# Optimization experiments

Hardware: AMD Instinct MI355X
Metric: run time of the kernel (lower is better)

The kernel has to match this reference:

```python
import jax, jax.numpy as jnp
import numpy as np

M, K, N = 8192, 4096, 4096  # tokens, in_features, out_features

def setup_inputs() -> dict:
    key = jax.random.key(0)
    k1, k2, k3 = jax.random.split(key, 3)
    x = jax.random.normal(k1, (M, K), dtype=jnp.float32)
    # kaiming_uniform_(a=sqrt(5)) on [out,in] -> uniform(-1/sqrt(in), 1/sqrt(in))
    bound = 1.0 / np.sqrt(K)
    weight = jax.random.uniform(k2, (N, K), dtype=jnp.float32, minval=-bound, maxval=bound)
    bias = jax.random.uniform(k3, (N,), dtype=jnp.float32, minval=-bound, maxval=bound)
    return {
        "x": x,
        "weight": weight,
        "bias": bias,
        "input_scale": jnp.float32(1.0),
        "weight_scale": jnp.float32(1.0),
    }


def reference(x, weight, bias, input_scale, weight_scale):
    # Quantize input and weight to fp8 e4m3 (per-tensor scale = 1.0 in module),
    # then dequant-matmul: out = (x_fp8 @ w_fp8^T) * scale_a * scale_b + bias,
    # matching torch._scaled_mm semantics with out_dtype=float32.
    x_fp8 = x.astype(jnp.float8_e4m3fn)
    w_fp8 = weight.astype(jnp.float8_e4m3fn)
    out = jnp.einsum(
        "mk,nk->mn",
        x_fp8.astype(jnp.float32),
        w_fp8.astype(jnp.float32),
    ) * (input_scale * weight_scale)
    return out + bias[None, :]
```

## Files before the change

### kernel.cpp

```cpp
#include <hip/hip_runtime.h>
#include <hip/hip_fp8.h>
#include <cstdint>

typedef float f32x4 __attribute__((ext_vector_type(4)));
typedef int i32x8 __attribute__((ext_vector_type(8)));
typedef long long i64;

static constexpr int Mdim = 8192;
static constexpr int Kdim = 4096;
static constexpr int Ndim = 4096;

static constexpr int BM = 256, BN = 256, BK = 128;
static constexpr int NT = Kdim / BK;
static constexpr int NWG_M = Mdim / BM;
static constexpr int NWG_N = Ndim / BN;
static constexpr int NWG = NWG_M * NWG_N;


__device__ __forceinline__ uint8_t f32_to_e4m3(float f) {
  return (uint8_t)__hip_cvt_float_to_fp8(f, __HIP_SATFINITE, __HIP_E4M3);
}

__device__ __forceinline__ uint4 cvt16(const float4 f0, const float4 f1,
                                       const float4 f2, const float4 f3) {
  const float v[16] = {f0.x, f0.y, f0.z, f0.w, f1.x, f1.y, f1.z, f1.w,
                       f2.x, f2.y, f2.z, f2.w, f3.x, f3.y, f3.z, f3.w};
  union alignas(16) {
    uint32_t u[4];
    uint8_t b[16];
    uint4 q;
  } r;
#pragma unroll
  for (int j = 0; j < 16; ++j) r.b[j] = f32_to_e4m3(v[j]);
  return r.q;
}

__global__ __launch_bounds__(256) void quant_fp8_kernel(
    const float* __restrict__ in, uint8_t* __restrict__ out, int n_vec16) {
  const int stride = gridDim.x * blockDim.x;
  for (int i = blockIdx.x * blockDim.x + threadIdx.x; i < n_vec16; i += stride) {
    const float4* src = reinterpret_cast<const float4*>(in) + (size_t)i * 4;
    reinterpret_cast<uint4*>(out)[i] = cvt16(src[0], src[1], src[2], src[3]);
  }
}

__global__ __launch_bounds__(256) void quant_pack_w_kernel(
    const float* __restrict__ W, uint8_t* __restrict__ PB) {
  const int stride = gridDim.x * blockDim.x;
  const int total = (Ndim / 16) * (Kdim / 16) * 16;
  for (int t = blockIdx.x * blockDim.x + threadIdx.x; t < total; t += stride) {
    const int g = t >> 8;
    const int kbi = t & 255;
    const int kt = kbi >> 3;
    const int kq = (kbi >> 1) & 3;
    const int h = kbi & 1;
    const int rb = g >> 4, r15 = g & 15;
    const float4* src =
        reinterpret_cast<const float4*>(W + (size_t)g * Kdim + kbi * 16);
    const size_t o = (((size_t)(rb * 32 + kt) * 2 + h) * 4 + kq) * 16 + r15;
    reinterpret_cast<uint4*>(PB)[o] = cvt16(src[0], src[1], src[2], src[3]);
  }
}

__device__ __forceinline__ void gload_lds16(const uint8_t* g, uint8_t* l) {
  __builtin_amdgcn_global_load_lds(
      (const __attribute__((address_space(1))) void*)g,
      (__attribute__((address_space(3))) void*)l, 16, 0, 0);
}

__device__ __forceinline__ f32x4 mx_mfma(i32x8 a, i32x8 b, f32x4 c) {
  return __builtin_amdgcn_mfma_scale_f32_16x16x128_f8f6f4(
      a, b, c, 0, 0, 0, 0x7f7f7f7f, 0, 0x7f7f7f7f);
}

__global__ __launch_bounds__(512, 2) void gemm_fp8_mx_pb(
    const uint8_t* __restrict__ Aq, const uint8_t* __restrict__ PB,
    const float* __restrict__ bias, const float* __restrict__ sa,
    const float* __restrict__ sb, float* __restrict__ C) {
  __shared__ alignas(16) uint8_t sA[2][BM * BK];

  const int wg = (int)blockIdx.x;
  const int xcd = wg & 7;
  const int within = wg >> 3;
  const int bn0 = (xcd * 2 + (within >> 5)) * BN;
  const int bm0 = (within & 31) * BM;

  const int t = (int)threadIdx.x;
  const int lane = t & 63;
  const int wave = t >> 6;
  const int wm = wave >> 2;
  const int wn = wave & 3;

  const int srow = t >> 3;
  const int sc16 = (t & 7) ^ (srow & 7);
  const uint8_t* aBase = Aq + (size_t)(bm0 + srow) * Kdim + sc16 * 16;
  const int ldsOff = t * 16;

  auto stageA = [&](int buf, int kt) {
    const size_t kb = (size_t)kt * BK;
#pragma unroll
    for (int i = 0; i < 4; ++i)
      gload_lds16(aBase + kb + (size_t)(i * 64) * Kdim,
                  &sA[buf][i * 8192 + ldsOff]);
  };

  const int r7 = lane & 7;
  const int kg = (lane >> 4) * 2;
  const int off0 = (kg ^ r7) * 16;
  const int off1 = ((kg + 1) ^ r7) * 16;
  const int rbA = (wm * 128 + (lane & 15)) * BK;

  auto ldfrag = [&](const uint8_t* base) -> i32x8 {
    union {
      i32x8 v;
      int4 h[2];
    } u;
    u.h[0] = *reinterpret_cast<const int4*>(base + off0);
    u.h[1] = *reinterpret_cast<const int4*>(base + off1);
    return u.v;
  };

  const int rbB0 = (bn0 >> 4) + wn * 4;
  auto ldb = [&](int n, int kt) -> i32x8 {
    const uint8_t* p =
        PB + ((size_t)((rbB0 + n) * 32 + kt) * 2048) + lane * 16;
    union {
      i32x8 v;
      int4 h[2];
    } u;
    u.h[0] = *reinterpret_cast<const int4*>(p);
    u.h[1] = *reinterpret_cast<const int4*>(p + 1024);
    return u.v;
  };

  f32x4 acc[8][4] = {};

  stageA(0, 0);
  asm volatile("s_waitcnt vmcnt(0)" ::: "memory");
  __builtin_amdgcn_s_barrier();

#pragma unroll 1
  for (int kt = 0; kt < NT; ++kt) {
    const int c = kt & 1;
    const uint8_t* A = &sA[c][0];

    i32x8 bf0 = ldb(0, kt);
    i32x8 bf1 = ldb(1, kt);
    i32x8 bf2 = ldb(2, kt);
    i32x8 bf3 = ldb(3, kt);

    if (kt + 1 < NT) stageA(c ^ 1, kt + 1);

    i32x8 a0 = ldfrag(A + rbA + 0 * 16 * BK);
    i32x8 a1 = ldfrag(A + rbA + 1 * 16 * BK);
    i32x8 a2 = ldfrag(A + rbA + 2 * 16 * BK);
    i32x8 a3 = ldfrag(A + rbA + 3 * 16 * BK);

    __builtin_amdgcn_s_setprio(1);
    acc[0][0] = mx_mfma(a0, bf0, acc[0][0]);
    acc[0][1] = mx_mfma(a0, bf1, acc[0][1]);
    acc[0][2] = mx_mfma(a0, bf2, acc[0][2]);
    acc[0][3] = mx_mfma(a0, bf3, acc[0][3]);
    acc[1][0] = mx_mfma(a1, bf0, acc[1][0]);
    acc[1][1] = mx_mfma(a1, bf1, acc[1][1]);
    acc[1][2] = mx_mfma(a1, bf2, acc[1][2]);
    acc[1][3] = mx_mfma(a1, bf3, acc[1][3]);
    __builtin_amdgcn_s_setprio(0);

    i32x8 a4 = ldfrag(A + rbA + 4 * 16 * BK);
    i32x8 a5 = ldfrag(A + rbA + 5 * 16 * BK);

    __builtin_amdgcn_s_setprio(1);
    acc[2][0] = mx_mfma(a2, bf0, acc[2][0]);
    acc[2][1] = mx_mfma(a2, bf1, acc[2][1]);
    acc[2][2] = mx_mfma(a2, bf2, acc[2][2]);
    acc[2][3] = mx_mfma(a2, bf3, acc[2][3]);
    acc[3][0] = mx_mfma(a3, bf0, acc[3][0]);
    acc[3][1] = mx_mfma(a3, bf1, acc[3][1]);
    acc[3][2] = mx_mfma(a3, bf2, acc[3][2]);
    acc[3][3] = mx_mfma(a3, bf3, acc[3][3]);
    __builtin_amdgcn_s_setprio(0);

    i32x8 a6 = ldfrag(A + rbA + 6 * 16 * BK);
    i32x8 a7 = ldfrag(A + rbA + 7 * 16 * BK);

    __builtin_amdgcn_s_setprio(1);
    acc[4][0] = mx_mfma(a4, bf0, acc[4][0]);
    acc[4][1] = mx_mfma(a4, bf1, acc[4][1]);
    acc[4][2] = mx_mfma(a4, bf2, acc[4][2]);
    acc[4][3] = mx_mfma(a4, bf3, acc[4][3]);
    acc[5][0] = mx_mfma(a5, bf0, acc[5][0]);
    acc[5][1] = mx_mfma(a5, bf1, acc[5][1]);
    acc[5][2] = mx_mfma(a5, bf2, acc[5][2]);
    acc[5][3] = mx_mfma(a5, bf3, acc[5][3]);
    __builtin_amdgcn_s_setprio(0);

    __builtin_amdgcn_s_setprio(1);
    acc[6][0] = mx_mfma(a6, bf0, acc[6][0]);
    acc[6][1] = mx_mfma(a6, bf1, acc[6][1]);
    acc[6][2] = mx_mfma(a6, bf2, acc[6][2]);
    acc[6][3] = mx_mfma(a6, bf3, acc[6][3]);
    acc[7][0] = mx_mfma(a7, bf0, acc[7][0]);
    acc[7][1] = mx_mfma(a7, bf1, acc[7][1]);
    acc[7][2] = mx_mfma(a7, bf2, acc[7][2]);
    acc[7][3] = mx_mfma(a7, bf3, acc[7][3]);
    __builtin_amdgcn_s_setprio(0);

    asm volatile("s_waitcnt vmcnt(0)" ::: "memory");
    __builtin_amdgcn_s_barrier();
  }

  const float scale = sa[0] * sb[0];
  const int orow0 = bm0 + wm * 128 + ((lane >> 4) << 2);
  const int ocol0 = bn0 + wn * 64 + (lane & 15);
#pragma unroll
  for (int n = 0; n < 4; ++n) {
    const int col = ocol0 + n * 16;
    const float bv = bias[col];
#pragma unroll
    for (int m = 0; m < 8; ++m) {
      const int row = orow0 + m * 16;
#pragma unroll
      for (int r = 0; r < 4; ++r)
        C[(size_t)(row + r) * Ndim + col] = acc[m][n][r] * scale + bv;
    }
  }
}

__device__ __forceinline__ void stage16_cvt(const float* g, uint8_t* l) {
  const float4* s = reinterpret_cast<const float4*>(g);
  uint4 q = cvt16(s[0], s[1], s[2], s[3]);
  *reinterpret_cast<uint4*>(l) = q;
}

__global__ __launch_bounds__(256) void gemm_fp8_fused_kernel(
    const float* __restrict__ X, const float* __restrict__ W,
    const float* __restrict__ bias, const float* __restrict__ sa,
    const float* __restrict__ sb, float* __restrict__ C) {
  constexpr int FBM = 128, FBN = 128, FBK = 64;
  constexpr int FNWG_N = Ndim / FBN;
  __shared__ alignas(16) uint8_t As[FBM * FBK];
  __shared__ alignas(16) uint8_t Bs[FBN * FBK];

  int wg = (int)blockIdx.x;
  const int nwg = (Mdim / FBM) * FNWG_N;
  wg = (wg & 7) * (nwg / 8) + (wg >> 3);
  const int bm0 = (wg / FNWG_N) * FBM;
  const int bn0 = (wg % FNWG_N) * FBN;

  const int t = (int)threadIdx.x;
  const int lane = t & 63;
  const int wave = t >> 6;
  const int wm = wave >> 1, wn = wave & 1;

  const int c0 = t, c1 = t + 256;
  const int r0 = c0 >> 2, col0 = (c0 & 3) * 16;
  const int r1 = c1 >> 2, col1 = (c1 & 3) * 16;
  const float* xa0 = X + (size_t)(bm0 + r0) * Kdim + col0;
  const float* xa1 = X + (size_t)(bm0 + r1) * Kdim + col1;
  const float* wb0 = W + (size_t)(bn0 + r0) * Kdim + col0;
  const float* wb1 = W + (size_t)(bn0 + r1) * Kdim + col1;

  const int arow = (wm * 64 + (lane & 15)) * FBK;
  const int brow = (wn * 64 + (lane & 15)) * FBK;
  const int koff = (lane >> 4) * 8;

  f32x4 acc[4][4] = {};

  for (int kt = 0; kt < Kdim / FBK; ++kt) {
    const int kb = kt * FBK;
    stage16_cvt(xa0 + kb, As + c0 * 16);
    stage16_cvt(xa1 + kb, As + c1 * 16);
    stage16_cvt(wb0 + kb, Bs + c0 * 16);
    stage16_cvt(wb1 + kb, Bs + c1 * 16);
    __syncthreads();
#pragma unroll
    for (int kk = 0; kk < FBK / 32; ++kk) {
      i64 a[4], b[4];
#pragma unroll
      for (int m = 0; m < 4; ++m)
        a[m] = *reinterpret_cast<const i64*>(&As[arow + m * 16 * FBK + kk * 32 + koff]);
#pragma unroll
      for (int n = 0; n < 4; ++n)
        b[n] = *reinterpret_cast<const i64*>(&Bs[brow + n * 16 * FBK + kk * 32 + koff]);
#pragma unroll
      for (int m = 0; m < 4; ++m)
#pragma unroll
        for (int n = 0; n < 4; ++n)
          acc[m][n] = __builtin_amdgcn_mfma_f32_16x16x32_fp8_fp8(
              a[m], b[n], acc[m][n], 0, 0, 0);
    }
    __syncthreads();
  }

  const float scale = sa[0] * sb[0];
  const int orow0 = bm0 + wm * 64 + ((lane >> 4) << 2);
  const int ocol0 = bn0 + wn * 64 + (lane & 15);
#pragma unroll
  for (int n = 0; n < 4; ++n) {
    const int col = ocol0 + n * 16;
    const float bv = bias[col];
#pragma unroll
    for (int m = 0; m < 4; ++m) {
      const int row = orow0 + m * 16;
#pragma unroll
      for (int r = 0; r < 4; ++r)
        C[(size_t)(row + r) * Ndim + col] = acc[m][n][r] * scale + bv;
    }
  }
}

extern "C" void kernel_launch(void* const* d_in, const int* in_sizes, int n_in,
                              void* d_out, int out_size, void* d_ws, size_t ws_size,
                              hipStream_t stream) {
  const float* x = (const float*)d_in[0];
  const float* w = (const float*)d_in[1];
  const float* bias = (const float*)d_in[2];
  const float* s_in = (const float*)d_in[3];
  const float* s_w = (const float*)d_in[4];
  float* out = (float*)d_out;

  const size_t needA = (size_t)Mdim * Kdim;
  const size_t needB = (size_t)Ndim * Kdim;

  if (ws_size >= needA + needB) {
    uint8_t* Aq = (uint8_t*)d_ws;
    uint8_t* PB = Aq + needA;
    quant_fp8_kernel<<<2048, 256, 0, stream>>>(x, Aq, (int)(needA / 16));
    quant_pack_w_kernel<<<2048, 256, 0, stream>>>(w, PB);
    gemm_fp8_mx_pb<<<NWG, 512, 0, stream>>>(Aq, PB, bias, s_in, s_w, out);
  } else {
    gemm_fp8_fused_kernel<<<(Mdim / 128) * (Ndim / 128), 256, 0, stream>>>(
        x, w, bias, s_in, s_w, out);
  }
}
```

Measured before the change: 216.2 us.

## Prefetch next-tile B fragments in registers during MFMAs; restructure weight pack grid

The GEMM loop now software-pipelines the B-operand global loads. The first tile's fragments load before the loop, and each iteration reloads bf0/bf1 and then bf2/bf3 for the next tile once their current uses finish, with the MFMAs reordered by B column to allow this. The end-of-iteration wait drops from vmcnt(0) to vmcnt(4), so the B prefetch can stay in flight across the barrier. The weight pack kernel switches from a grid-stride loop to one thread per 16-byte output chunk on a 4096-block grid, changing which source addresses neighbouring threads read. This risks higher register pressure and relies on vmcnt ordering being correct for the LDS staging of A.

```diff
diff --git a/kernel.cpp b/kernel.cpp
--- a/kernel.cpp
+++ b/kernel.cpp
@@ -46,20 +46,16 @@
 
 __global__ __launch_bounds__(256) void quant_pack_w_kernel(
     const float* __restrict__ W, uint8_t* __restrict__ PB) {
-  const int stride = gridDim.x * blockDim.x;
-  const int total = (Ndim / 16) * (Kdim / 16) * 16;
-  for (int t = blockIdx.x * blockDim.x + threadIdx.x; t < total; t += stride) {
-    const int g = t >> 8;
-    const int kbi = t & 255;
-    const int kt = kbi >> 3;
-    const int kq = (kbi >> 1) & 3;
-    const int h = kbi & 1;
-    const int rb = g >> 4, r15 = g & 15;
-    const float4* src =
-        reinterpret_cast<const float4*>(W + (size_t)g * Kdim + kbi * 16);
-    const size_t o = (((size_t)(rb * 32 + kt) * 2 + h) * 4 + kq) * 16 + r15;
-    reinterpret_cast<uint4*>(PB)[o] = cvt16(src[0], src[1], src[2], src[3]);
-  }
+  const int pair = blockIdx.x * 2 + ((int)threadIdx.x >> 7);
+  const int j = (int)threadIdx.x & 127;
+  const int rb = pair >> 5;
+  const int kt = pair & 31;
+  const int r15 = j & 15, kq = (j >> 4) & 3, h = j >> 6;
+  const int g = rb * 16 + r15;
+  const float4* src = reinterpret_cast<const float4*>(
+      W + (size_t)g * Kdim + kt * 128 + kq * 32 + h * 16);
+  const size_t o = (((size_t)(rb * 32 + kt) * 2 + h) * 4 + kq) * 16 + r15;
+  reinterpret_cast<uint4*>(PB)[o] = cvt16(src[0], src[1], src[2], src[3]);
 }
 
 __device__ __forceinline__ void gload_lds16(const uint8_t* g, uint8_t* l) {
@@ -73,7 +69,7 @@
       a, b, c, 0, 0, 0, 0x7f7f7f7f, 0, 0x7f7f7f7f);
 }
 
-__global__ __launch_bounds__(512, 2) void gemm_fp8_mx_pb(
+__global__ __launch_bounds__(512, 2) void gemm_fp8_mx_pf(
     const uint8_t* __restrict__ Aq, const uint8_t* __restrict__ PB,
     const float* __restrict__ bias, const float* __restrict__ sa,
     const float* __restrict__ sb, float* __restrict__ C) {
@@ -122,8 +118,7 @@
 
   const int rbB0 = (bn0 >> 4) + wn * 4;
   auto ldb = [&](int n, int kt) -> i32x8 {
-    const uint8_t* p =
-        PB + ((size_t)((rbB0 + n) * 32 + kt) * 2048) + lane * 16;
+    const uint8_t* p = PB + ((size_t)((rbB0 + n) * 32 + kt) * 2048) + lane * 16;
     union {
       i32x8 v;
       int4 h[2];
@@ -136,6 +131,10 @@
   f32x4 acc[8][4] = {};
 
   stageA(0, 0);
+  i32x8 bf0 = ldb(0, 0);
+  i32x8 bf1 = ldb(1, 0);
+  i32x8 bf2 = ldb(2, 0);
+  i32x8 bf3 = ldb(3, 0);
   asm volatile("s_waitcnt vmcnt(0)" ::: "memory");
   __builtin_amdgcn_s_barrier();
 
@@ -143,71 +142,71 @@
   for (int kt = 0; kt < NT; ++kt) {
     const int c = kt & 1;
     const uint8_t* A = &sA[c][0];
-
-    i32x8 bf0 = ldb(0, kt);
-    i32x8 bf1 = ldb(1, kt);
-    i32x8 bf2 = ldb(2, kt);
-    i32x8 bf3 = ldb(3, kt);
-
-    if (kt + 1 < NT) stageA(c ^ 1, kt + 1);
+    const bool more = (kt + 1 < NT);
+
+    if (more) stageA(c ^ 1, kt + 1);
 
     i32x8 a0 = ldfrag(A + rbA + 0 * 16 * BK);
     i32x8 a1 = ldfrag(A + rbA + 1 * 16 * BK);
     i32x8 a2 = ldfrag(A + rbA + 2 * 16 * BK);
     i32x8 a3 = ldfrag(A + rbA + 3 * 16 * BK);
-
     __builtin_amdgcn_s_setprio(1);
     acc[0][0] = mx_mfma(a0, bf0, acc[0][0]);
     acc[0][1] = mx_mfma(a0, bf1, acc[0][1]);
-    acc[0][2] = mx_mfma(a0, bf2, acc[0][2]);
-    acc[0][3] = mx_mfma(a0, bf3, acc[0][3]);
     acc[1][0] = mx_mfma(a1, bf0, acc[1][0]);
     acc[1][1] = mx_mfma(a1, bf1, acc[1][1]);
-    acc[1][2] = mx_mfma(a1, bf2, acc[1][2]);
-    acc[1][3] = mx_mfma(a1, bf3, acc[1][3]);
     __builtin_amdgcn_s_setprio(0);
-
     i32x8 a4 = ldfrag(A + rbA + 4 * 16 * BK);
     i32x8 a5 = ldfrag(A + rbA + 5 * 16 * BK);
-
     __builtin_amdgcn_s_setprio(1);
     acc[2][0] = mx_mfma(a2, bf0, acc[2][0]);
     acc[2][1] = mx_mfma(a2, bf1, acc[2][1]);
-    acc[2][2] = mx_mfma(a2, bf2, acc[2][2]);
-    acc[2][3] = mx_mfma(a2, bf3, acc[2][3]);
     acc[3][0] = mx_mfma(a3, bf0, acc[3][0]);
     acc[3][1] = mx_mfma(a3, bf1, acc[3][1]);
-    acc[3][2] = mx_mfma(a3, bf2, acc[3][2]);
-    acc[3][3] = mx_mfma(a3, bf3, acc[3][3]);
     __builtin_amdgcn_s_setprio(0);
-
     i32x8 a6 = ldfrag(A + rbA + 6 * 16 * BK);
     i32x8 a7 = ldfrag(A + rbA + 7 * 16 * BK);
-
     __builtin_amdgcn_s_setprio(1);
     acc[4][0] = mx_mfma(a4, bf0, acc[4][0]);
     acc[4][1] = mx_mfma(a4, bf1, acc[4][1]);
+    acc[5][0] = mx_mfma(a5, bf0, acc[5][0]);
+    acc[5][1] = mx_mfma(a5, bf1, acc[5][1]);
+    acc[6][0] = mx_mfma(a6, bf0, acc[6][0]);
+    acc[6][1] = mx_mfma(a6, bf1, acc[6][1]);
+    acc[7][0] = mx_mfma(a7, bf0, acc[7][0]);
+    acc[7][1] = mx_mfma(a7, bf1, acc[7][1]);
+    __builtin_amdgcn_s_setprio(0);
+
+    if (more) {
+      bf0 = ldb(0, kt + 1);
+      bf1 = ldb(1, kt + 1);
+    }
+
+    __builtin_amdgcn_s_setprio(1);
+    acc[0][2] = mx_mfma(a0, bf2, acc[0][2]);
+    acc[0][3] = mx_mfma(a0, bf3, acc[0][3]);
+    acc[1][2] = mx_mfma(a1, bf2, acc[1][2]);
+    acc[1][3] = mx_mfma(a1, bf3, acc[1][3]);
+    acc[2][2] = mx_mfma(a2, bf2, acc[2][2]);
+    acc[2][3] = mx_mfma(a2, bf3, acc[2][3]);
+    acc[3][2] = mx_mfma(a3, bf2, acc[3][2]);
+    acc[3][3] = mx_mfma(a3, bf3, acc[3][3]);
     acc[4][2] = mx_mfma(a4, bf2, acc[4][2]);
     acc[4][3] = mx_mfma(a4, bf3, acc[4][3]);
-    acc[5][0] = mx_mfma(a5, bf0, acc[5][0]);
-    acc[5][1] = mx_mfma(a5, bf1, acc[5][1]);
     acc[5][2] = mx_mfma(a5, bf2, acc[5][2]);
     acc[5][3] = mx_mfma(a5, bf3, acc[5][3]);
-    __builtin_amdgcn_s_setprio(0);
-
-    __builtin_amdgcn_s_setprio(1);
-    acc[6][0] = mx_mfma(a6, bf0, acc[6][0]);
-    acc[6][1] = mx_mfma(a6, bf1, acc[6][1]);
     acc[6][2] = mx_mfma(a6, bf2, acc[6][2]);
     acc[6][3] = mx_mfma(a6, bf3, acc[6][3]);
-    acc[7][0] = mx_mfma(a7, bf0, acc[7][0]);
-    acc[7][1] = mx_mfma(a7, bf1, acc[7][1]);
     acc[7][2] = mx_mfma(a7, bf2, acc[7][2]);
     acc[7][3] = mx_mfma(a7, bf3, acc[7][3]);
     __builtin_amdgcn_s_setprio(0);
 
-    asm volatile("s_waitcnt vmcnt(0)" ::: "memory");
-    __builtin_amdgcn_s_barrier();
+    if (more) {
+      bf2 = ldb(2, kt + 1);
+      bf3 = ldb(3, kt + 1);
+      asm volatile("s_waitcnt vmcnt(4)" ::: "memory");
+      __builtin_amdgcn_s_barrier();
+    }
   }
 
   const float scale = sa[0] * sb[0];
@@ -327,8 +326,8 @@
     uint8_t* Aq = (uint8_t*)d_ws;
     uint8_t* PB = Aq + needA;
     quant_fp8_kernel<<<2048, 256, 0, stream>>>(x, Aq, (int)(needA / 16));
-    quant_pack_w_kernel<<<2048, 256, 0, stream>>>(w, PB);
-    gemm_fp8_mx_pb<<<NWG, 512, 0, stream>>>(Aq, PB, bias, s_in, s_w, out);
+    quant_pack_w_kernel<<<4096, 256, 0, stream>>>(w, PB);
+    gemm_fp8_mx_pf<<<NWG, 512, 0, stream>>>(Aq, PB, bias, s_in, s_w, out);
   } else {
     gemm_fp8_fused_kernel<<<(Mdim / 128) * (Ndim / 128), 256, 0, stream>>>(
         x, w, bias, s_in, s_w, out);
```

After: 271.7 us. +25.7%, slower.
